# Kernel optimization log

Measured on AMD Instinct MI355X. Metric: run time of the kernel, lower is better.

## Reference

```python
import jax, jax.numpy as jnp
import numpy as np

EPS = 1e-08


def setup_inputs() -> dict:
    key = jax.random.key(0)
    k1, k2 = jax.random.split(key)
    query_features = jax.random.normal(k1, (64, 1024, 32, 32), dtype=jnp.float32)
    support_features = jax.random.normal(k2, (25, 1024, 32, 32), dtype=jnp.float32)
    return {"query_features": query_features, "support_features": support_features}


def reference(query_features, support_features):
    B, C, h, w = support_features.shape
    NQ = query_features.shape[0]
    # Covariance over channels: flatten support to (C, B*h*w), center, GEMM.
    support = jnp.transpose(support_features, (1, 0, 2, 3)).reshape(C, -1)
    centered = support - jnp.mean(support, axis=1, keepdims=True)
    N = B * h * w
    cov = (centered @ centered.T) / (N - 1 + EPS)  # (C, C)
    # Queries: (NQ, C, d), L2-normalize each channel row over spatial dim.
    q = query_features.reshape(NQ, C, -1)
    q = q / (jnp.linalg.norm(q, axis=2, keepdims=True) + EPS)
    # diag(q^T cov q) without materializing (d, d): cov@q then elementwise reduce over C.
    cq = jnp.einsum('cD,nDd->ncd', cov, q)  # (NQ, C, d)
    scores = jnp.mean(jnp.sum(q * cq, axis=1), axis=1)  # (NQ,)
    return scores
```

## Files before the change

kernel.cpp:

```cpp
#include <hip/hip_runtime.h>

#define NQ   64
#define CCH  1024
#define DSP  1024
#define NSUP 25600
#define KSLICES 8
#define NK_COV 50

typedef __attribute__((ext_vector_type(4))) float f32x4;
typedef __attribute__((ext_vector_type(8))) __bf16 bf16x8;

#define WAITVM(N) asm volatile("s_waitcnt vmcnt(" #N ")" ::: "memory")
#define WAITLGKM0() asm volatile("s_waitcnt lgkmcnt(0)" ::: "memory")

__device__ inline unsigned short f2bf(float x) {
  unsigned u = __builtin_bit_cast(unsigned, x);
  u += 0x7fffu + ((u >> 16) & 1u);
  return (unsigned short)(u >> 16);
}

__global__ __launch_bounds__(256) void zero_kernel(float4* __restrict__ cov4,
                                                   float4* __restrict__ out4) {
  const int i = blockIdx.x * 256 + threadIdx.x;
  cov4[i] = make_float4(0.f, 0.f, 0.f, 0.f);
  if (i < 16) out4[i] = make_float4(0.f, 0.f, 0.f, 0.f);
}


__global__ __launch_bounds__(256) void mean_center_kernel(
    const float* __restrict__ sup, float* __restrict__ mean,
    unsigned short* __restrict__ Sb, int write_sb) {
  const int c = blockIdx.x;
  const int tid = threadIdx.x;
  float s = 0.f;
  for (int qd = tid; qd < 6400; qd += 256) {
    const int b = qd >> 8, s4 = (qd & 255) << 2;
    const float4 v = *(const float4*)(sup + ((size_t)b * CCH + c) * DSP + s4);
    s += v.x + v.y + v.z + v.w;
  }
  __shared__ float red[256];
  red[tid] = s;
  __syncthreads();
  for (int st = 128; st > 0; st >>= 1) {
    if (tid < st) red[tid] += red[tid + st];
    __syncthreads();
  }
  const float m = red[0] * (1.0f / 25600.0f);
  if (tid == 0) mean[c] = m;
  if (write_sb) {
    for (int qd = tid; qd < 6400; qd += 256) {
      const int b = qd >> 8, s4 = (qd & 255) << 2;
      const float4 v = *(const float4*)(sup + ((size_t)b * CCH + c) * DSP + s4);
      ushort4 o;
      o.x = f2bf(v.x - m); o.y = f2bf(v.y - m);
      o.z = f2bf(v.z - m); o.w = f2bf(v.w - m);
      *(ushort4*)(Sb + (size_t)c * NSUP + b * DSP + s4) = o;
    }
  }
}

__global__ __launch_bounds__(256) void qnorm_kernel(
    const float* __restrict__ q, float* __restrict__ qfac,
    unsigned short* __restrict__ Qb, int write_qb) {
  const int row = blockIdx.x * 4 + (threadIdx.x >> 6);
  const int l = threadIdx.x & 63;
  const float4* src = (const float4*)(q + (size_t)row * DSP);
  float4 v[4];
  float ss = 0.f;
#pragma unroll
  for (int i = 0; i < 4; ++i) {
    v[i] = src[l + 64 * i];
    ss += v[i].x * v[i].x + v[i].y * v[i].y + v[i].z * v[i].z + v[i].w * v[i].w;
  }
#pragma unroll
  for (int off = 32; off > 0; off >>= 1) ss += __shfl_xor(ss, off);
  const float f = 1.0f / (sqrtf(ss) + 1e-8f);
  if (l == 0) qfac[row] = f;
  if (write_qb) {
#pragma unroll
    for (int i = 0; i < 4; ++i) {
      ushort4 o;
      o.x = f2bf(v[i].x * f); o.y = f2bf(v[i].y * f);
      o.z = f2bf(v[i].z * f); o.w = f2bf(v[i].w * f);
      *(ushort4*)(Qb + (size_t)row * DSP + (size_t)(l + 64 * i) * 4) = o;
    }
  }
}


__device__ inline void stage_glds(const unsigned short* __restrict__ src, int ld,
                                  int row0, int k0, unsigned short* lds) {
  const int tid = threadIdx.x;
  const int w = tid >> 6;
#pragma unroll
  for (int it = 0; it < 4; ++it) {
    const int ci = it * 256 + tid;
    const int r = ci >> 3;
    const int kc = ((ci & 7) ^ (r & 7)) << 3;
    const unsigned short* g = src + (size_t)(row0 + r) * ld + k0 + kc;
    unsigned short* lb = lds + ((it * 256 + w * 64) << 3);
    __builtin_amdgcn_global_load_lds((const __attribute__((address_space(1))) void*)g,
                                     (__attribute__((address_space(3))) void*)lb,
                                     16, 0, 0);
  }
}

__device__ inline void stage_sup_f32(const float* __restrict__ sup,
                                     const float* __restrict__ mean,
                                     int row0, int k0, unsigned short* lds) {
  const int tid = threadIdx.x;
#pragma unroll
  for (int it = 0; it < 4; ++it) {
    const int ci = it * 256 + tid;
    const int r = ci >> 3, kc = (ci & 7) << 3;
    const int c = row0 + r;
    const int k = k0 + kc;
    const int b = k >> 10, sp = k & 1023;
    const float4* g = (const float4*)(sup + ((size_t)b * CCH + c) * DSP + sp);
    const float4 v0 = g[0], v1 = g[1];
    const float m = mean[c];
    union { unsigned short h[8]; int4 q; } pk;
    pk.h[0] = f2bf(v0.x - m); pk.h[1] = f2bf(v0.y - m);
    pk.h[2] = f2bf(v0.z - m); pk.h[3] = f2bf(v0.w - m);
    pk.h[4] = f2bf(v1.x - m); pk.h[5] = f2bf(v1.y - m);
    pk.h[6] = f2bf(v1.z - m); pk.h[7] = f2bf(v1.w - m);
    *(int4*)(lds + (size_t)(r * 8 + ((ci & 7) ^ (r & 7))) * 8) = pk.q;
  }
}

__device__ inline void stage_q_f32(const float* __restrict__ qn,
                                   const float* __restrict__ qfacn,
                                   int row0, int k0, unsigned short* lds) {
  const int tid = threadIdx.x;
#pragma unroll
  for (int it = 0; it < 4; ++it) {
    const int ci = it * 256 + tid;
    const int r = ci >> 3, kc = (ci & 7) << 3;
    const int c = row0 + r;
    const float4* g = (const float4*)(qn + (size_t)c * DSP + k0 + kc);
    const float4 v0 = g[0], v1 = g[1];
    const float f = qfacn[c];
    union { unsigned short h[8]; int4 q; } pk;
    pk.h[0] = f2bf(v0.x * f); pk.h[1] = f2bf(v0.y * f);
    pk.h[2] = f2bf(v0.z * f); pk.h[3] = f2bf(v0.w * f);
    pk.h[4] = f2bf(v1.x * f); pk.h[5] = f2bf(v1.y * f);
    pk.h[6] = f2bf(v1.z * f); pk.h[7] = f2bf(v1.w * f);
    *(int4*)(lds + (size_t)(r * 8 + ((ci & 7) ^ (r & 7))) * 8) = pk.q;
  }
}

__device__ inline void compute_step(const unsigned short* lA, const unsigned short* lB,
                                    int wr, int wc, int lr, int kg, f32x4 acc[4][4]) {
  const int sc = (lr & 7) << 3;
  __builtin_amdgcn_s_setprio(1);
#pragma unroll
  for (int kk = 0; kk < 64; kk += 32) {
    const int col = (kk + kg) ^ sc;
    bf16x8 a[4], b[4];
#pragma unroll
    for (int i = 0; i < 4; ++i)
      a[i] = *(const bf16x8*)(const void*)(lA + (wr + i * 16 + lr) * 64 + col);
#pragma unroll
    for (int j = 0; j < 4; ++j)
      b[j] = *(const bf16x8*)(const void*)(lB + (wc + j * 16 + lr) * 64 + col);
#pragma unroll
    for (int i = 0; i < 4; ++i)
#pragma unroll
      for (int j = 0; j < 4; ++j)
        acc[i][j] = __builtin_amdgcn_mfma_f32_16x16x32_bf16(a[i], b[j], acc[i][j], 0, 0, 0);
  }
  __builtin_amdgcn_s_setprio(0);
}

__device__ inline void pre_compute_sync_nondiag() {
  WAITVM(8);
  __builtin_amdgcn_s_barrier();
  __builtin_amdgcn_sched_barrier(0);
}
__device__ inline void pre_compute_sync_diag() {
  WAITVM(4);
  __builtin_amdgcn_s_barrier();
  __builtin_amdgcn_sched_barrier(0);
}
__device__ inline void pre_compute_sync_last() {
  WAITVM(0);
  __builtin_amdgcn_s_barrier();
  __builtin_amdgcn_sched_barrier(0);
}
__device__ inline void post_compute_sync() {
  WAITLGKM0();
  __builtin_amdgcn_s_barrier();
  __builtin_amdgcn_sched_barrier(0);
}

__device__ inline void decode_tile(int t, int& ti, int& tj) {
  int rem = t; ti = 0;
  while (rem >= 8 - ti) { rem -= 8 - ti; ++ti; }
  tj = ti + rem;
}

template <bool F32>
__global__ __launch_bounds__(256) void cov_kernel(
    const unsigned short* __restrict__ Sb, const float* __restrict__ sup,
    const float* __restrict__ mean, float* __restrict__ cov) {
  __shared__ unsigned short lA[2][128 * 64];
  __shared__ unsigned short lB[2][128 * 64];
  const int wg = blockIdx.x;
  const int ks = wg & 7;
  int ti, tj; decode_tile(wg >> 3, ti, tj);
  const bool diag = (ti == tj);
  const int tid = threadIdx.x, l = tid & 63, w = tid >> 6;
  const int wr = (w >> 1) * 64, wc = (w & 1) * 64, lr = l & 15, kg = (l >> 4) * 8;
  f32x4 acc[4][4];
#pragma unroll
  for (int i = 0; i < 4; ++i)
#pragma unroll
    for (int j = 0; j < 4; ++j) acc[i][j] = 0.f;

  const int kbase = ks * (NSUP / KSLICES);

  if (F32) {
    stage_sup_f32(sup, mean, ti * 128, kbase, lA[0]);
    if (!diag) stage_sup_f32(sup, mean, tj * 128, kbase, lB[0]);
    __syncthreads();
    int cur = 0;
    for (int kt = 0; kt < NK_COV; ++kt) {
      if (kt + 1 < NK_COV) {
        const int k1 = kbase + (kt + 1) * 64;
        stage_sup_f32(sup, mean, ti * 128, k1, lA[cur ^ 1]);
        if (!diag) stage_sup_f32(sup, mean, tj * 128, k1, lB[cur ^ 1]);
      }
      compute_step(lA[cur], diag ? lA[cur] : lB[cur], wr, wc, lr, kg, acc);
      __syncthreads();
      cur ^= 1;
    }
  } else {
    stage_glds(Sb, NSUP, ti * 128, kbase, lA[0]);
    if (!diag) stage_glds(Sb, NSUP, tj * 128, kbase, lB[0]);
    int cur = 0;
    for (int kt = 0; kt < NK_COV; ++kt) {
      if (kt + 1 < NK_COV) {
        const int k1 = kbase + (kt + 1) * 64;
        stage_glds(Sb, NSUP, ti * 128, k1, lA[cur ^ 1]);
        if (!diag) {
          stage_glds(Sb, NSUP, tj * 128, k1, lB[cur ^ 1]);
          pre_compute_sync_nondiag();
        } else {
          pre_compute_sync_diag();
        }
      } else {
        pre_compute_sync_last();
      }
      compute_step(lA[cur], diag ? lA[cur] : lB[cur], wr, wc, lr, kg, acc);
      post_compute_sync();
      cur ^= 1;
    }
  }

  const float scale = 1.0f / (25599.0f + 1e-8f);
  const int rbase = ti * 128 + wr + (l >> 4) * 4;
  const int cbase = tj * 128 + wc + (l & 15);
#pragma unroll
  for (int i = 0; i < 4; ++i)
#pragma unroll
    for (int j = 0; j < 4; ++j)
#pragma unroll
      for (int r = 0; r < 4; ++r)
        atomicAdd(&cov[(size_t)(rbase + i * 16 + r) * CCH + cbase + j * 16],
                  acc[i][j][r] * scale);
}

template <bool F32>
__global__ __launch_bounds__(256) void gram_kernel(
    const unsigned short* __restrict__ Qb, const float* __restrict__ q,
    const float* __restrict__ qfac, const float* __restrict__ cov,
    float* __restrict__ out) {
  __shared__ unsigned short lA[2][128 * 64];
  __shared__ unsigned short lB[2][128 * 64];
  const int wg = blockIdx.x;
  const int xcd = wg & 7, slot = wg >> 3;
  const int n = xcd * 8 + slot / 36;
  int ti, tj; decode_tile(slot % 36, ti, tj);
  const bool diag = (ti == tj);
  const int tid = threadIdx.x, l = tid & 63, w = tid >> 6;
  const int wr = (w >> 1) * 64, wc = (w & 1) * 64, lr = l & 15, kg = (l >> 4) * 8;
  f32x4 acc[4][4];
#pragma unroll
  for (int i = 0; i < 4; ++i)
#pragma unroll
    for (int j = 0; j < 4; ++j) acc[i][j] = 0.f;

  const unsigned short* Qn = Qb + (size_t)n * CCH * DSP;
  const float* qn = q + (size_t)n * CCH * DSP;
  const float* qfacn = qfac + (size_t)n * CCH;

  if (F32) {
    stage_q_f32(qn, qfacn, ti * 128, 0, lA[0]);
    if (!diag) stage_q_f32(qn, qfacn, tj * 128, 0, lB[0]);
    __syncthreads();
    int cur = 0;
    for (int kt = 0; kt < 16; ++kt) {
      if (kt + 1 < 16) {
        const int k1 = (kt + 1) * 64;
        stage_q_f32(qn, qfacn, ti * 128, k1, lA[cur ^ 1]);
        if (!diag) stage_q_f32(qn, qfacn, tj * 128, k1, lB[cur ^ 1]);
      }
      compute_step(lA[cur], diag ? lA[cur] : lB[cur], wr, wc, lr, kg, acc);
      __syncthreads();
      cur ^= 1;
    }
  } else {
    stage_glds(Qn, DSP, ti * 128, 0, lA[0]);
    if (!diag) stage_glds(Qn, DSP, tj * 128, 0, lB[0]);
    int cur = 0;
    for (int kt = 0; kt < 16; ++kt) {
      if (kt + 1 < 16) {
        const int k1 = (kt + 1) * 64;
        stage_glds(Qn, DSP, ti * 128, k1, lA[cur ^ 1]);
        if (!diag) {
          stage_glds(Qn, DSP, tj * 128, k1, lB[cur ^ 1]);
          pre_compute_sync_nondiag();
        } else {
          pre_compute_sync_diag();
        }
      } else {
        pre_compute_sync_last();
      }
      compute_step(lA[cur], diag ? lA[cur] : lB[cur], wr, wc, lr, kg, acc);
      post_compute_sync();
      cur ^= 1;
    }
  }

  float s = 0.f;
  const int rbase = ti * 128 + wr + (l >> 4) * 4;
  const int cbase = tj * 128 + wc + (l & 15);
#pragma unroll
  for (int i = 0; i < 4; ++i)
#pragma unroll
    for (int j = 0; j < 4; ++j)
#pragma unroll
      for (int r = 0; r < 4; ++r)
        s += acc[i][j][r] * cov[(size_t)(rbase + i * 16 + r) * CCH + cbase + j * 16];
  if (!diag) s *= 2.0f;
  s *= (1.0f / 1024.0f);
#pragma unroll
  for (int off = 32; off > 0; off >>= 1) s += __shfl_xor(s, off);
  if (l == 0) atomicAdd(&out[n], s);
}

extern "C" void kernel_launch(void* const* d_in, const int* in_sizes, int n_in,
                              void* d_out, int out_size, void* d_ws, size_t ws_size,
                              hipStream_t stream) {
  const float* q = (const float*)d_in[0];
  const float* sup = (const float*)d_in[1];
  float* out = (float*)d_out;

  char* ws = (char*)d_ws;
  float* mean = (float*)ws;
  float* qfac = (float*)(ws + (4 << 10));
  float* cov  = (float*)(ws + (4 << 10) + (256 << 10));
  unsigned short* Sb = (unsigned short*)(ws + (4 << 10) + (256 << 10) + (4 << 20));
  unsigned short* Qb = Sb + (size_t)CCH * NSUP;
  const size_t need_fat = (size_t)(4 << 10) + (256 << 10) + (4 << 20) +
                          (size_t)CCH * NSUP * 2 + (size_t)NQ * CCH * DSP * 2;
  const bool fat = ws_size >= need_fat;

  zero_kernel<<<1024, 256, 0, stream>>>((float4*)cov, (float4*)out);

  mean_center_kernel<<<CCH, 256, 0, stream>>>(sup, mean, Sb, fat ? 1 : 0);
  qnorm_kernel<<<NQ * CCH / 4, 256, 0, stream>>>(q, qfac, Qb, fat ? 1 : 0);

  if (fat) {
    cov_kernel<false><<<dim3(288), 256, 0, stream>>>(Sb, sup, mean, cov);
    gram_kernel<false><<<dim3(8 * 8 * 36), 256, 0, stream>>>(Qb, q, qfac, cov, out);
  } else {
    cov_kernel<true><<<dim3(288), 256, 0, stream>>>(Sb, sup, mean, cov);
    gram_kernel<true><<<dim3(8 * 8 * 36), 256, 0, stream>>>(Qb, q, qfac, cov, out);
  }
}
```

Baseline: 303.6 us.

## Replace per-query Gram kernel with 256x256-tile, 8-wave bf16 MFMA kernel

Adds gram256_kernel, which computes each query's symmetric Q·Qᵀ Gram matrix in 256x256 upper-triangular tiles (10 per query) with 512-thread blocks, double-buffered global_load_lds staging and XOR-swizzled LDS. Larger tiles halve the global/LDS traffic per MFMA relative to the old 128x128 tiles and cut the block count from 2304 to 640. The trade-offs are 128 KB of LDS per block, which limits occupancy, extra barriers interleaved between MFMA groups, and more diagonal-tile work wasted on symmetric halves. The fat path now launches the new kernel, and the old kernel's bf16 branch is removed, leaving only its f32 path.

```diff
diff --git a/kernel.cpp b/kernel.cpp
--- a/kernel.cpp
+++ b/kernel.cpp
@@ -12,6 +12,7 @@
 
 #define WAITVM(N) asm volatile("s_waitcnt vmcnt(" #N ")" ::: "memory")
 #define WAITLGKM0() asm volatile("s_waitcnt lgkmcnt(0)" ::: "memory")
+#define BAR() __builtin_amdgcn_s_barrier()
 
 __device__ inline unsigned short f2bf(float x) {
   unsigned u = __builtin_bit_cast(unsigned, x);
@@ -173,24 +174,16 @@
 }
 
 __device__ inline void pre_compute_sync_nondiag() {
-  WAITVM(8);
-  __builtin_amdgcn_s_barrier();
-  __builtin_amdgcn_sched_barrier(0);
+  WAITVM(8); BAR(); __builtin_amdgcn_sched_barrier(0);
 }
 __device__ inline void pre_compute_sync_diag() {
-  WAITVM(4);
-  __builtin_amdgcn_s_barrier();
-  __builtin_amdgcn_sched_barrier(0);
+  WAITVM(4); BAR(); __builtin_amdgcn_sched_barrier(0);
 }
 __device__ inline void pre_compute_sync_last() {
-  WAITVM(0);
-  __builtin_amdgcn_s_barrier();
-  __builtin_amdgcn_sched_barrier(0);
+  WAITVM(0); BAR(); __builtin_amdgcn_sched_barrier(0);
 }
 __device__ inline void post_compute_sync() {
-  WAITLGKM0();
-  __builtin_amdgcn_s_barrier();
-  __builtin_amdgcn_sched_barrier(0);
+  WAITLGKM0(); BAR(); __builtin_amdgcn_sched_barrier(0);
 }
 
 __device__ inline void decode_tile(int t, int& ti, int& tj) {
@@ -290,46 +283,22 @@
 #pragma unroll
     for (int j = 0; j < 4; ++j) acc[i][j] = 0.f;
 
-  const unsigned short* Qn = Qb + (size_t)n * CCH * DSP;
   const float* qn = q + (size_t)n * CCH * DSP;
   const float* qfacn = qfac + (size_t)n * CCH;
 
-  if (F32) {
-    stage_q_f32(qn, qfacn, ti * 128, 0, lA[0]);
-    if (!diag) stage_q_f32(qn, qfacn, tj * 128, 0, lB[0]);
+  stage_q_f32(qn, qfacn, ti * 128, 0, lA[0]);
+  if (!diag) stage_q_f32(qn, qfacn, tj * 128, 0, lB[0]);
+  __syncthreads();
+  int cur = 0;
+  for (int kt = 0; kt < 16; ++kt) {
+    if (kt + 1 < 16) {
+      const int k1 = (kt + 1) * 64;
+      stage_q_f32(qn, qfacn, ti * 128, k1, lA[cur ^ 1]);
+      if (!diag) stage_q_f32(qn, qfacn, tj * 128, k1, lB[cur ^ 1]);
+    }
+    compute_step(lA[cur], diag ? lA[cur] : lB[cur], wr, wc, lr, kg, acc);
     __syncthreads();
-    int cur = 0;
-    for (int kt = 0; kt < 16; ++kt) {
-      if (kt + 1 < 16) {
-        const int k1 = (kt + 1) * 64;
-        stage_q_f32(qn, qfacn, ti * 128, k1, lA[cur ^ 1]);
-        if (!diag) stage_q_f32(qn, qfacn, tj * 128, k1, lB[cur ^ 1]);
-      }
-      compute_step(lA[cur], diag ? lA[cur] : lB[cur], wr, wc, lr, kg, acc);
-      __syncthreads();
-      cur ^= 1;
-    }
-  } else {
-    stage_glds(Qn, DSP, ti * 128, 0, lA[0]);
-    if (!diag) stage_glds(Qn, DSP, tj * 128, 0, lB[0]);
-    int cur = 0;
-    for (int kt = 0; kt < 16; ++kt) {
-      if (kt + 1 < 16) {
-        const int k1 = (kt + 1) * 64;
-        stage_glds(Qn, DSP, ti * 128, k1, lA[cur ^ 1]);
-        if (!diag) {
-          stage_glds(Qn, DSP, tj * 128, k1, lB[cur ^ 1]);
-          pre_compute_sync_nondiag();
-        } else {
-          pre_compute_sync_diag();
-        }
-      } else {
-        pre_compute_sync_last();
-      }
-      compute_step(lA[cur], diag ? lA[cur] : lB[cur], wr, wc, lr, kg, acc);
-      post_compute_sync();
-      cur ^= 1;
-    }
+    cur ^= 1;
   }
 
   float s = 0.f;
@@ -343,6 +312,115 @@
       for (int r = 0; r < 4; ++r)
         s += acc[i][j][r] * cov[(size_t)(rbase + i * 16 + r) * CCH + cbase + j * 16];
   if (!diag) s *= 2.0f;
+  s *= (1.0f / 1024.0f);
+#pragma unroll
+  for (int off = 32; off > 0; off >>= 1) s += __shfl_xor(s, off);
+  if (l == 0) atomicAdd(&out[n], s);
+}
+
+
+__device__ inline void stage256(const unsigned short* __restrict__ src,
+                                int row0, int k0, unsigned short* lds_base) {
+  const int tid = threadIdx.x;
+  const int wid = tid >> 6;
+#pragma unroll
+  for (int it = 0; it < 4; ++it) {
+    const int ci = it * 512 + tid;
+    const int r = ci >> 3;
+    const int kc = ((ci & 7) ^ (r & 7)) << 3;
+    const unsigned short* g = src + (size_t)(row0 + r) * DSP + k0 + kc;
+    unsigned short* lb = lds_base + ((it * 512 + (wid << 6)) << 3);
+    __builtin_amdgcn_global_load_lds((const __attribute__((address_space(1))) void*)g,
+                                     (__attribute__((address_space(3))) void*)lb,
+                                     16, 0, 0);
+  }
+}
+
+__device__ inline void rd_a4(const unsigned short* A, int q, int col, int lr, bf16x8 a[4]) {
+#pragma unroll
+  for (int i = 0; i < 4; ++i)
+    a[i] = *(const bf16x8*)(const void*)(A + (q * 64 + i * 16 + lr) * 64 + col);
+}
+__device__ inline void rd_b4(const unsigned short* B, int brow, int col, int lr, bf16x8 b[4]) {
+#pragma unroll
+  for (int j = 0; j < 4; ++j)
+    b[j] = *(const bf16x8*)(const void*)(B + (brow + j * 16 + lr) * 64 + col);
+}
+__device__ inline void mfma16(const bf16x8 a[4], const bf16x8 b[4], f32x4 (*acc)[4]) {
+  __builtin_amdgcn_s_setprio(1);
+#pragma unroll
+  for (int i = 0; i < 4; ++i)
+#pragma unroll
+    for (int j = 0; j < 4; ++j)
+      acc[i][j] = __builtin_amdgcn_mfma_f32_16x16x32_bf16(a[i], b[j], acc[i][j], 0, 0, 0);
+  __builtin_amdgcn_s_setprio(0);
+}
+
+__global__ __launch_bounds__(512, 2) void gram256_kernel(
+    const unsigned short* __restrict__ Qb, const float* __restrict__ cov,
+    float* __restrict__ out) {
+  __shared__ unsigned short lds[65536];
+  const int wg = blockIdx.x;
+  const int xcd = wg & 7, slot = wg >> 3;
+  const int n = xcd * 8 + slot / 10;
+  int rem = slot % 10, ti = 0;
+  while (rem >= 4 - ti) { rem -= 4 - ti; ++ti; }
+  const int tj = ti + rem;
+  const int tid = threadIdx.x, l = tid & 63, wid = tid >> 6;
+  const int wm = wid >> 2, wn = wid & 3;
+  const int lr = l & 15, kg = (l >> 4) * 8;
+  const int sw = (lr & 7) << 3;
+  const unsigned short* Qn = Qb + (size_t)n * CCH * DSP;
+
+  f32x4 acc[8][4];
+#pragma unroll
+  for (int i = 0; i < 8; ++i)
+#pragma unroll
+    for (int j = 0; j < 4; ++j) acc[i][j] = 0.f;
+
+  stage256(Qn, ti * 256, 0, lds);
+  stage256(Qn, tj * 256, 0, lds + 16384);
+  WAITVM(0);
+  BAR();
+
+  for (int t = 0; t < 16; ++t) {
+    const int cb = (t & 1) << 15;
+    if (t < 15) {
+      const int nb = cb ^ 32768;
+      stage256(Qn, ti * 256, (t + 1) * 64, lds + nb);
+      stage256(Qn, tj * 256, (t + 1) * 64, lds + nb + 16384);
+    }
+    const unsigned short* A = lds + cb + wm * 8192;
+    const unsigned short* B = lds + cb + 16384 + (wn >> 1) * 8192;
+    const int brow = (wn & 1) * 64;
+    bf16x8 a[4], b[4];
+#pragma unroll
+    for (int kk = 0; kk < 64; kk += 32) {
+      const int col = (kk + kg) ^ sw;
+      rd_b4(B, brow, col, lr, b);
+      rd_a4(A, 0, col, lr, a);
+      BAR();
+      mfma16(a, b, &acc[0]);
+      BAR();
+      rd_a4(A, 1, col, lr, a);
+      BAR();
+      mfma16(a, b, &acc[4]);
+      if (kk == 32 && t < 15) WAITVM(0);
+      BAR();
+    }
+  }
+
+  float s = 0.f;
+  const int rbase = ti * 256 + wm * 128 + (l >> 4) * 4;
+  const int cbase = tj * 256 + wn * 64 + (l & 15);
+#pragma unroll
+  for (int i = 0; i < 8; ++i)
+#pragma unroll
+    for (int j = 0; j < 4; ++j)
+#pragma unroll
+      for (int r = 0; r < 4; ++r)
+        s += acc[i][j][r] * cov[(size_t)(rbase + i * 16 + r) * CCH + cbase + j * 16];
+  if (ti != tj) s *= 2.0f;
   s *= (1.0f / 1024.0f);
 #pragma unroll
   for (int off = 32; off > 0; off >>= 1) s += __shfl_xor(s, off);
@@ -373,7 +451,7 @@
 
   if (fat) {
     cov_kernel<false><<<dim3(288), 256, 0, stream>>>(Sb, sup, mean, cov);
-    gram_kernel<false><<<dim3(8 * 8 * 36), 256, 0, stream>>>(Qb, q, qfac, cov, out);
+    gram256_kernel<<<dim3(640), 512, 0, stream>>>(Qb, cov, out);
   } else {
     cov_kernel<true><<<dim3(288), 256, 0, stream>>>(Sb, sup, mean, cov);
     gram_kernel<true><<<dim3(8 * 8 * 36), 256, 0, stream>>>(Qb, q, qfac, cov, out);
```

Result: no change. 301.9 us (-0.6%).
